# Optimization experiments

Measured on AMD Instinct MI355X. Metric: run time of the kernel, lower is better.

Reference implementation:

```python
import jax, jax.numpy as jnp
import numpy as np

B, S, D = 8, 1024, 768
H = 12
HD = D // H
DROPOUT_P = 0.5


def setup_inputs() -> dict:
    key = jax.random.key(0)
    ks = jax.random.split(key, 9)
    scale = 1.0 / np.sqrt(D)
    return {
        "x": jax.random.normal(ks[0], (B, S, D), dtype=jnp.float32),
        "wq": jax.random.normal(ks[1], (D, D), dtype=jnp.float32) * scale,
        "bq": jax.random.normal(ks[2], (D,), dtype=jnp.float32) * 0.01,
        "wk": jax.random.normal(ks[3], (D, D), dtype=jnp.float32) * scale,
        "bk": jax.random.normal(ks[4], (D,), dtype=jnp.float32) * 0.01,
        "wv": jax.random.normal(ks[5], (D, D), dtype=jnp.float32) * scale,
        "bv": jax.random.normal(ks[6], (D,), dtype=jnp.float32) * 0.01,
        "wo": jax.random.normal(ks[7], (D, D), dtype=jnp.float32) * scale,
        "bo": jax.random.normal(ks[8], (D,), dtype=jnp.float32) * 0.01,
    }


def reference(x, wq, bq, wk, bk, wv, bv, wo, bo):
    # QKV projections (torch Linear: y = x @ W.T + b)
    def proj(w, b):
        y = jnp.einsum("bsd,ed->bse", x, w) + b
        # [B,S,D] -> [B,H,S,HD]
        return y.reshape(B, S, H, HD).transpose(0, 2, 1, 3)

    q = proj(wq, bq)
    k = proj(wk, bk)
    v = proj(wv, bv)

    scores = jnp.einsum("bhqd,bhkd->bhqk", q, k) / jnp.sqrt(
        jnp.asarray(HD, dtype=x.dtype)
    )
    # dropout BEFORE softmax (non-standard, faithful to source), training=True
    dkey = jax.random.key(42)
    keep = jax.random.bernoulli(dkey, 1.0 - DROPOUT_P, scores.shape)
    scores = jnp.where(keep, scores / (1.0 - DROPOUT_P), 0.0)

    attn = jax.nn.softmax(scores, axis=-1)
    o = jnp.einsum("bhqk,bhkd->bhqd", attn, v)
    o = o.transpose(0, 2, 1, 3).reshape(B, S, D)
    return jnp.einsum("bsd,ed->bse", o, wo) + bo
```

## Files before the change

kernel.cpp:

```cpp
#include <hip/hip_runtime.h>
#include <hip/hip_bf16.h>
#include <stdint.h>

typedef __bf16 bf16_t;
typedef __attribute__((ext_vector_type(8))) __bf16 bf16x8;
typedef __attribute__((ext_vector_type(4))) __bf16 bf16x4;
typedef __attribute__((ext_vector_type(4))) float f32x4;

#define MFMA16(a, b, c) __builtin_amdgcn_mfma_f32_16x16x32_bf16(a, b, c, 0, 0, 0)

#define KS2 (0x1BD11BDAu ^ 42u)
#define OFF_TILES 9
#define GMASK_WORDS 1769472u

#define ROT4(rr)                                                        \
    {                                                                   \
        y00 += y10; y10 = __builtin_amdgcn_alignbit(y10, y10, 32u - (rr)); y10 ^= y00; \
        y01 += y11; y11 = __builtin_amdgcn_alignbit(y11, y11, 32u - (rr)); y11 ^= y01; \
        y02 += y12; y12 = __builtin_amdgcn_alignbit(y12, y12, 32u - (rr)); y12 ^= y02; \
        y03 += y13; y13 = __builtin_amdgcn_alignbit(y13, y13, 32u - (rr)); y13 ^= y03; \
    }
#define INJ4(a, b)                                                      \
    {                                                                   \
        y00 += (a); y10 += (b);                                         \
        y01 += (a); y11 += (b);                                         \
        y02 += (a); y12 += (b);                                         \
        y03 += (a); y13 += (b);                                         \
    }

__device__ __forceinline__ uint32_t tf4bits(uint32_t e0, int c) {
    uint32_t y00 = 0u, y10 = e0 + 42u;
    uint32_t y01 = 0u, y11 = e0 + 43u;
    uint32_t y02 = 0u, y12 = e0 + 44u;
    uint32_t y03 = 0u, y13 = e0 + 45u;
    ROT4(13) ROT4(15) ROT4(26) ROT4(6)   INJ4(42u, KS2 + 1u)
    ROT4(17) ROT4(29) ROT4(16) ROT4(24)  INJ4(KS2, 0u + 2u)
    ROT4(13) ROT4(15) ROT4(26) ROT4(6)   INJ4(0u, 42u + 3u)
    ROT4(17) ROT4(29) ROT4(16) ROT4(24)  INJ4(42u, KS2 + 4u)
    ROT4(13) ROT4(15) ROT4(26) ROT4(6)   INJ4(KS2, 0u + 5u)
    const uint32_t b0 = (y00 ^ y10) >> 31, b1 = (y01 ^ y11) >> 31;
    const uint32_t b2 = (y02 ^ y12) >> 31, b3 = (y03 ^ y13) >> 31;
    return (b0 | (b1 << 1) | (b2 << 2) | (b3 << 3)) << c;
}

__device__ __forceinline__ bf16x8 cvt8(float4 a, float4 b) {
    bf16x8 v;
    v[0] = (bf16_t)a.x; v[1] = (bf16_t)a.y; v[2] = (bf16_t)a.z; v[3] = (bf16_t)a.w;
    v[4] = (bf16_t)b.x; v[5] = (bf16_t)b.y; v[6] = (bf16_t)b.z; v[7] = (bf16_t)b.w;
    return v;
}

__global__ __launch_bounds__(512, 4)
void qkv_gemm(const float* __restrict__ x,
              const float* __restrict__ wq, const float* __restrict__ bq,
              const float* __restrict__ wk, const float* __restrict__ bk,
              const float* __restrict__ wv, const float* __restrict__ bv,
              bf16_t* __restrict__ qb, bf16_t* __restrict__ kb,
              bf16_t* __restrict__ vtb, uint32_t* __restrict__ gmask)
{
    const int mt = blockIdx.x;
    const int nt = blockIdx.y;
    const int mat = blockIdx.z;

    __shared__ bf16_t As[128][40];
    __shared__ bf16_t Bs[128][40];

    const int t = threadIdx.x;

    if (t < 256) {
        const float* w   = (mat == 0) ? wq : ((mat == 1) ? wk : wv);
        const float* bia = (mat == 0) ? bq : ((mat == 1) ? bk : bv);
        const int wid = t >> 6, l = t & 63, l15 = l & 15, lg = l >> 4;
        const int wr = wid >> 1, wc = wid & 1;

        f32x4 acc[4][4] = {};
        const int srow = t >> 1, scol = (t & 1) * 16;
        const float* xa = x + (size_t)(mt * 128 + srow) * 768 + scol;
        const float* wa = w + (size_t)(nt * 128 + srow) * 768 + scol;

        for (int kt = 0; kt < 24; ++kt) {
            const float* pa = xa + kt * 32;
            const float* pb = wa + kt * 32;
            float4 a0 = *(const float4*)(pa + 0),  a1 = *(const float4*)(pa + 4);
            float4 a2 = *(const float4*)(pa + 8),  a3 = *(const float4*)(pa + 12);
            float4 b0 = *(const float4*)(pb + 0),  b1 = *(const float4*)(pb + 4);
            float4 b2 = *(const float4*)(pb + 8),  b3 = *(const float4*)(pb + 12);
            __syncthreads();
            *(bf16x8*)&As[srow][scol]     = cvt8(a0, a1);
            *(bf16x8*)&As[srow][scol + 8] = cvt8(a2, a3);
            *(bf16x8*)&Bs[srow][scol]     = cvt8(b0, b1);
            *(bf16x8*)&Bs[srow][scol + 8] = cvt8(b2, b3);
            __syncthreads();

            bf16x8 af[4], bf[4];
#pragma unroll
            for (int m = 0; m < 4; ++m) af[m] = *(const bf16x8*)&As[wr * 64 + m * 16 + l15][lg * 8];
#pragma unroll
            for (int n = 0; n < 4; ++n) bf[n] = *(const bf16x8*)&Bs[wc * 64 + n * 16 + l15][lg * 8];
#pragma unroll
            for (int m = 0; m < 4; ++m)
#pragma unroll
                for (int n = 0; n < 4; ++n)
                    acc[m][n] = MFMA16(af[m], bf[n], acc[m][n]);
        }

        const int eb = nt * 128 + wc * 64;
        const int mb = mt * 128 + wr * 64;
#pragma unroll
        for (int n = 0; n < 4; ++n) {
            const int e = eb + n * 16 + l15;
            const float bias = bia[e];
            const int h = e >> 6, hd = e & 63;
#pragma unroll
            for (int m = 0; m < 4; ++m) {
                const int m0 = mb + m * 16 + lg * 4;
                const int b = m0 >> 10, s0 = m0 & 1023;
                if (mat == 2) {
                    bf16x4 pv;
#pragma unroll
                    for (int r = 0; r < 4; ++r) pv[r] = (bf16_t)(acc[m][n][r] + bias);
                    *(bf16x4*)(vtb + (((size_t)(b * 12 + h)) << 16) + ((size_t)hd << 10) + s0) = pv;
                } else {
                    bf16_t* dst = (mat == 0) ? qb : kb;
                    const float sc = (mat == 0) ? 0.25f : 1.0f;
                    const size_t base = (((size_t)(b * 12 + h)) << 16) + ((size_t)s0 << 6) + hd;
#pragma unroll
                    for (int r = 0; r < 4; ++r)
                        dst[base + (size_t)r * 64] = (bf16_t)((acc[m][n][r] + bias) * sc);
                }
            }
        }
    } else {
        const uint32_t u = (uint32_t)(t - 256);
        const uint32_t bl = (uint32_t)(mt + 64 * (nt + 6 * mat));
        const uint32_t wbase = bl * 1536u + u;
        uint32_t word = 0u, ebase = 0u, widx = 0u;
        for (int s = 0; s < 48; ++s) {
            const int chunk = s >> 3, c = (s & 7) * 4;
            if ((s & 7) == 0) {
                widx = wbase + 256u * (uint32_t)chunk;
                const uint32_t bh  = widx / 18432u;
                const uint32_t rem = widx - bh * 18432u;
                const uint32_t q   = rem / 18u;
                const uint32_t w18 = rem - q * 18u;
                ebase = (bh << 20) | (q << 10) | (w18 * 32u);
                word = 0u;
            }
            word |= tf4bits(ebase + (uint32_t)c, c);
            if ((s & 7) == 7) gmask[widx] = word;
            __syncthreads();
        }
    }
}

__global__ __launch_bounds__(512, 4)
void attn_kernel(const bf16_t* __restrict__ qb, const bf16_t* __restrict__ kb,
                 const bf16_t* __restrict__ vtb, const uint32_t* __restrict__ gmask,
                 bf16_t* __restrict__ ob)
{
    const int qt = blockIdx.x;
    const int bh = blockIdx.y;
    const int t = threadIdx.x, w = t >> 6, l = t & 63, l15 = l & 15, lg = l >> 4;

    __shared__ bf16_t Kl[2][64][72];
    __shared__ bf16_t Vl[2][64][72];
    __shared__ bf16_t Pl[4][16][72];
    __shared__ ushort Mh[7][64][2][2];

    const size_t base = ((size_t)bh) << 16;
    const uint32_t fbase = ((uint32_t)bh) << 20;
    const int q0b = qt * 64;
    const int q0 = q0b + w * 16;

    const int u = t & 255;
    const int mq = u >> 2, mword = (u >> 1) & 1, mhalf = u & 1;
    const uint32_t moff = (uint32_t)(mword * 32 + mhalf * 16);

    f32x4 oacc[4] = {};
    float lst[4] = {0.f, 0.f, 0.f, 0.f};
    bf16x8 qf[2];
    uint32_t mhw = 0u;
    int ms = 0;

    if (w < 4) {
        const size_t qbase = base + (size_t)(q0 + l15) * 64 + lg * 8;
        qf[0] = *(const bf16x8*)(qb + qbase);
        qf[1] = *(const bf16x8*)(qb + qbase + 32);
#pragma unroll
        for (int sdx = 0; sdx < 2; ++sdx) {
            const int idx = sdx * 256 + t;
            const int row = idx >> 3, seg = idx & 7;
            *(uint4*)&Kl[0][row][seg * 8] =
                *(const uint4*)(kb + base + ((size_t)row << 6) + seg * 8);
            *(uint4*)&Vl[0][row][seg * 8] =
                *(const uint4*)(vtb + base + ((size_t)row << 10) + seg * 8);
        }
    }
    __syncthreads();

    for (int kt = 0; kt < 16; ++kt) {
        const int cur = kt & 1, nxt = cur ^ 1;
        if (w < 4) {
            const int ktn = (kt < 15) ? kt + 1 : 15;
            const int row0 = t >> 3, seg = t & 7;
            const int row1 = row0 + 32;
            const uint4 ka0 = *(const uint4*)(kb + base + ((size_t)(ktn * 64 + row0) << 6) + seg * 8);
            const uint4 ka1 = *(const uint4*)(kb + base + ((size_t)(ktn * 64 + row1) << 6) + seg * 8);
            const uint4 va0 = *(const uint4*)(vtb + base + ((size_t)row0 << 10) + ktn * 64 + seg * 8);
            const uint4 va1 = *(const uint4*)(vtb + base + ((size_t)row1 << 10) + ktn * 64 + seg * 8);

            f32x4 sc[4] = {};
#pragma unroll
            for (int ks = 0; ks < 2; ++ks)
#pragma unroll
                for (int n = 0; n < 4; ++n) {
                    bf16x8 kf = *(const bf16x8*)&Kl[cur][n * 16 + l15][ks * 32 + lg * 8];
                    sc[n] = MFMA16(qf[ks], kf, sc[n]);
                }

#pragma unroll
            for (int r = 0; r < 4; ++r) {
                const int ql = w * 16 + lg * 4 + r;
                uint32_t w0, w1;
                if (kt < OFF_TILES) {
                    const uint32_t qg = (uint32_t)(q0b + ql);
                    const uint32_t wi = ((uint32_t)bh * 1024u + qg) * 18u + (uint32_t)(kt * 2);
                    w0 = gmask[wi]; w1 = gmask[wi + 1];
                } else {
                    const uint32_t* mrow = (const uint32_t*)&Mh[kt - OFF_TILES][ql][0][0];
                    w0 = mrow[0]; w1 = mrow[1];
                }
                float ps = 0.f;
#pragma unroll
                for (int n = 0; n < 4; ++n) {
                    const uint32_t wrd = (n < 2) ? w0 : w1;
                    const uint32_t bit = ((uint32_t)(n & 1) << 4) + (uint32_t)l15;
                    const float e = __expf(sc[n][r]);
                    const float p = ((wrd >> bit) & 1u) ? 1.0f : e;
                    ps += p;
                    Pl[w][lg * 4 + r][n * 16 + l15] = (bf16_t)p;
                }
                lst[r] += ps;
            }

            {
                const bf16x8 pa0 = *(const bf16x8*)&Pl[w][l15][lg * 8];
                const bf16x8 pa1 = *(const bf16x8*)&Pl[w][l15][32 + lg * 8];
#pragma unroll
                for (int n = 0; n < 4; ++n) {
                    const bf16x8 v0 = *(const bf16x8*)&Vl[cur][n * 16 + l15][lg * 8];
                    const bf16x8 v1 = *(const bf16x8*)&Vl[cur][n * 16 + l15][32 + lg * 8];
                    oacc[n] = MFMA16(pa0, v0, oacc[n]);
                    oacc[n] = MFMA16(pa1, v1, oacc[n]);
                }
            }

            {
                const int row0w = t >> 3, segw = t & 7;
                *(uint4*)&Kl[nxt][row0w][segw * 8]      = ka0;
                *(uint4*)&Kl[nxt][row0w + 32][segw * 8] = ka1;
                *(uint4*)&Vl[nxt][row0w][segw * 8]      = va0;
                *(uint4*)&Vl[nxt][row0w + 32][segw * 8] = va1;
            }
        } else {
#pragma unroll
            for (int q2 = 0; q2 < 2; ++q2) {
                if (ms < 28) {
                    const int ti = ms >> 2;
                    const int c = (ms & 3) * 4;
                    const uint32_t mbase = fbase | ((uint32_t)(q0b + mq) << 10)
                                         | ((uint32_t)((OFF_TILES + ti) * 64) + moff + (uint32_t)c);
                    mhw |= tf4bits(mbase, c);
                    if ((ms & 3) == 3) {
                        Mh[ti][mq][mword][mhalf] = (ushort)mhw;
                        mhw = 0u;
                    }
                    ++ms;
                }
            }
        }
        __syncthreads();
    }

    if (w < 4) {
        const int b = bh / 12, h = bh % 12;
#pragma unroll
        for (int r = 0; r < 4; ++r) {
            float ps = lst[r];
#pragma unroll
            for (int mk = 1; mk < 16; mk <<= 1) ps += __shfl_xor(ps, mk);
            const float inv = 1.f / ps;
            const size_t row = ((size_t)(b * 1024 + q0 + lg * 4 + r)) * 768 + h * 64;
#pragma unroll
            for (int n = 0; n < 4; ++n)
                ob[row + n * 16 + l15] = (bf16_t)(oacc[n][r] * inv);
        }
    }
}

__global__ __launch_bounds__(256, 2)
void out_gemm(const bf16_t* __restrict__ ob, const float* __restrict__ wo,
              const float* __restrict__ bo, float* __restrict__ out)
{
    const int mt = blockIdx.x, nt = blockIdx.y;
    __shared__ bf16_t As[128][40];
    __shared__ bf16_t Bs[128][40];
    const int t = threadIdx.x;
    const int wid = t >> 6, l = t & 63, l15 = l & 15, lg = l >> 4;
    const int wr = wid >> 1, wc = wid & 1;
    f32x4 acc[4][4] = {};

    const int srow = t >> 1, scol = (t & 1) * 16;
    const bf16_t* aa = ob + (size_t)(mt * 128 + srow) * 768 + scol;
    const float*  wa = wo + (size_t)(nt * 128 + srow) * 768 + scol;

    for (int kt = 0; kt < 24; ++kt) {
        uint4 a01 = *(const uint4*)(aa + kt * 32);
        uint4 a23 = *(const uint4*)(aa + kt * 32 + 8);
        const float* pb = wa + kt * 32;
        float4 b0 = *(const float4*)(pb + 0), b1 = *(const float4*)(pb + 4);
        float4 b2 = *(const float4*)(pb + 8), b3 = *(const float4*)(pb + 12);
        __syncthreads();
        *(uint4*)&As[srow][scol]      = a01;
        *(uint4*)&As[srow][scol + 8]  = a23;
        *(bf16x8*)&Bs[srow][scol]     = cvt8(b0, b1);
        *(bf16x8*)&Bs[srow][scol + 8] = cvt8(b2, b3);
        __syncthreads();

        bf16x8 af[4], bf[4];
#pragma unroll
        for (int m = 0; m < 4; ++m) af[m] = *(const bf16x8*)&As[wr * 64 + m * 16 + l15][lg * 8];
#pragma unroll
        for (int n = 0; n < 4; ++n) bf[n] = *(const bf16x8*)&Bs[wc * 64 + n * 16 + l15][lg * 8];
#pragma unroll
        for (int m = 0; m < 4; ++m)
#pragma unroll
            for (int n = 0; n < 4; ++n)
                acc[m][n] = MFMA16(af[m], bf[n], acc[m][n]);
    }

#pragma unroll
    for (int n = 0; n < 4; ++n) {
        const int e = nt * 128 + wc * 64 + n * 16 + l15;
        const float bias = bo[e];
#pragma unroll
        for (int m = 0; m < 4; ++m) {
            const int m0 = mt * 128 + wr * 64 + m * 16 + lg * 4;
#pragma unroll
            for (int r = 0; r < 4; ++r)
                out[(size_t)(m0 + r) * 768 + e] = acc[m][n][r] + bias;
        }
    }
}

__global__ void fill_zero(float* p, int n) {
    int i = blockIdx.x * 256 + threadIdx.x;
    if (i < n) p[i] = 0.f;
}

extern "C" void kernel_launch(void* const* d_in, const int* in_sizes, int n_in,
                              void* d_out, int out_size, void* d_ws, size_t ws_size,
                              hipStream_t stream) {
    const float* x  = (const float*)d_in[0];
    const float* wq = (const float*)d_in[1];
    const float* bq = (const float*)d_in[2];
    const float* wk = (const float*)d_in[3];
    const float* bk = (const float*)d_in[4];
    const float* wv = (const float*)d_in[5];
    const float* bv = (const float*)d_in[6];
    const float* wo = (const float*)d_in[7];
    const float* bo = (const float*)d_in[8];
    float* out = (float*)d_out;

    const size_t NEED = 4ull * 6291456ull * 2ull + (size_t)GMASK_WORDS * 4ull;
    if (ws_size < NEED) {
        fill_zero<<<(out_size + 255) / 256, 256, 0, stream>>>(out, out_size);
        return;
    }

    bf16_t* qb  = (bf16_t*)d_ws;
    bf16_t* kb  = qb  + 6291456;
    bf16_t* vtb = kb  + 6291456;
    bf16_t* ob  = vtb + 6291456;
    uint32_t* gmask = (uint32_t*)(ob + 6291456);

    qkv_gemm<<<dim3(64, 6, 3), 512, 0, stream>>>(x, wq, bq, wk, bk, wv, bv,
                                                 qb, kb, vtb, gmask);
    attn_kernel<<<dim3(16, 96), 512, 0, stream>>>(qb, kb, vtb, gmask, ob);
    out_gemm<<<dim3(64, 6), 256, 0, stream>>>(ob, wo, bo, out);
}
```

Measured before the change: 274.0 us.

## Double-buffer QKV GEMM shared tiles and halve barriers per k-step

After: 275.9 us. Within noise of the previous version (+0.7%).

```diff
diff --git a/kernel.cpp b/kernel.cpp
--- a/kernel.cpp
+++ b/kernel.cpp
@@ -62,8 +62,8 @@
     const int nt = blockIdx.y;
     const int mat = blockIdx.z;
 
-    __shared__ bf16_t As[128][40];
-    __shared__ bf16_t Bs[128][40];
+    __shared__ bf16_t As[2][128][40];
+    __shared__ bf16_t Bs[2][128][40];
 
     const int t = threadIdx.x;
 
@@ -78,30 +78,49 @@
         const float* xa = x + (size_t)(mt * 128 + srow) * 768 + scol;
         const float* wa = w + (size_t)(nt * 128 + srow) * 768 + scol;
 
+        {
+            float4 a0 = *(const float4*)(xa + 0),  a1 = *(const float4*)(xa + 4);
+            float4 a2 = *(const float4*)(xa + 8),  a3 = *(const float4*)(xa + 12);
+            float4 b0 = *(const float4*)(wa + 0),  b1 = *(const float4*)(wa + 4);
+            float4 b2 = *(const float4*)(wa + 8),  b3 = *(const float4*)(wa + 12);
+            *(bf16x8*)&As[0][srow][scol]     = cvt8(a0, a1);
+            *(bf16x8*)&As[0][srow][scol + 8] = cvt8(a2, a3);
+            *(bf16x8*)&Bs[0][srow][scol]     = cvt8(b0, b1);
+            *(bf16x8*)&Bs[0][srow][scol + 8] = cvt8(b2, b3);
+        }
+
         for (int kt = 0; kt < 24; ++kt) {
-            const float* pa = xa + kt * 32;
-            const float* pb = wa + kt * 32;
-            float4 a0 = *(const float4*)(pa + 0),  a1 = *(const float4*)(pa + 4);
-            float4 a2 = *(const float4*)(pa + 8),  a3 = *(const float4*)(pa + 12);
-            float4 b0 = *(const float4*)(pb + 0),  b1 = *(const float4*)(pb + 4);
-            float4 b2 = *(const float4*)(pb + 8),  b3 = *(const float4*)(pb + 12);
             __syncthreads();
-            *(bf16x8*)&As[srow][scol]     = cvt8(a0, a1);
-            *(bf16x8*)&As[srow][scol + 8] = cvt8(a2, a3);
-            *(bf16x8*)&Bs[srow][scol]     = cvt8(b0, b1);
-            *(bf16x8*)&Bs[srow][scol + 8] = cvt8(b2, b3);
-            __syncthreads();
+            const int cur = kt & 1;
+
+            float4 a0, a1, a2, a3, b0, b1, b2, b3;
+            if (kt < 23) {
+                const float* pa = xa + (kt + 1) * 32;
+                const float* pb = wa + (kt + 1) * 32;
+                a0 = *(const float4*)(pa + 0);  a1 = *(const float4*)(pa + 4);
+                a2 = *(const float4*)(pa + 8);  a3 = *(const float4*)(pa + 12);
+                b0 = *(const float4*)(pb + 0);  b1 = *(const float4*)(pb + 4);
+                b2 = *(const float4*)(pb + 8);  b3 = *(const float4*)(pb + 12);
+            }
 
             bf16x8 af[4], bf[4];
 #pragma unroll
-            for (int m = 0; m < 4; ++m) af[m] = *(const bf16x8*)&As[wr * 64 + m * 16 + l15][lg * 8];
-#pragma unroll
-            for (int n = 0; n < 4; ++n) bf[n] = *(const bf16x8*)&Bs[wc * 64 + n * 16 + l15][lg * 8];
+            for (int m = 0; m < 4; ++m) af[m] = *(const bf16x8*)&As[cur][wr * 64 + m * 16 + l15][lg * 8];
+#pragma unroll
+            for (int n = 0; n < 4; ++n) bf[n] = *(const bf16x8*)&Bs[cur][wc * 64 + n * 16 + l15][lg * 8];
 #pragma unroll
             for (int m = 0; m < 4; ++m)
 #pragma unroll
                 for (int n = 0; n < 4; ++n)
                     acc[m][n] = MFMA16(af[m], bf[n], acc[m][n]);
+
+            if (kt < 23) {
+                const int nb = cur ^ 1;
+                *(bf16x8*)&As[nb][srow][scol]     = cvt8(a0, a1);
+                *(bf16x8*)&As[nb][srow][scol + 8] = cvt8(a2, a3);
+                *(bf16x8*)&Bs[nb][srow][scol]     = cvt8(b0, b1);
+                *(bf16x8*)&Bs[nb][srow][scol + 8] = cvt8(b2, b3);
+            }
         }
 
         const int eb = nt * 128 + wc * 64;
@@ -135,20 +154,24 @@
         const uint32_t bl = (uint32_t)(mt + 64 * (nt + 6 * mat));
         const uint32_t wbase = bl * 1536u + u;
         uint32_t word = 0u, ebase = 0u, widx = 0u;
-        for (int s = 0; s < 48; ++s) {
-            const int chunk = s >> 3, c = (s & 7) * 4;
-            if ((s & 7) == 0) {
-                widx = wbase + 256u * (uint32_t)chunk;
-                const uint32_t bh  = widx / 18432u;
-                const uint32_t rem = widx - bh * 18432u;
-                const uint32_t q   = rem / 18u;
-                const uint32_t w18 = rem - q * 18u;
-                ebase = (bh << 20) | (q << 10) | (w18 * 32u);
-                word = 0u;
-            }
-            word |= tf4bits(ebase + (uint32_t)c, c);
-            if ((s & 7) == 7) gmask[widx] = word;
+        for (int it = 0; it < 24; ++it) {
             __syncthreads();
+#pragma unroll
+            for (int q2 = 0; q2 < 2; ++q2) {
+                const int s = it * 2 + q2;
+                const int chunk = s >> 3, c = (s & 7) * 4;
+                if ((s & 7) == 0) {
+                    widx = wbase + 256u * (uint32_t)chunk;
+                    const uint32_t bh  = widx / 18432u;
+                    const uint32_t rem = widx - bh * 18432u;
+                    const uint32_t q   = rem / 18u;
+                    const uint32_t w18 = rem - q * 18u;
+                    ebase = (bh << 20) | (q << 10) | (w18 * 32u);
+                    word = 0u;
+                }
+                word |= tf4bits(ebase + (uint32_t)c, c);
+                if ((s & 7) == 7) gmask[widx] = word;
+            }
         }
     }
 }
```

## Split mask generation into separate blocks instead of sharing blocks with GEMM waves

Applied to the files above, without the earlier changes.

After: 551.1 us. +101.1%, slower.

```diff
diff --git a/kernel.cpp b/kernel.cpp
--- a/kernel.cpp
+++ b/kernel.cpp
@@ -50,105 +50,102 @@
     return v;
 }
 
-__global__ __launch_bounds__(512, 4)
-void qkv_gemm(const float* __restrict__ x,
+__global__ __launch_bounds__(256)
+void qkv_mask(const float* __restrict__ x,
               const float* __restrict__ wq, const float* __restrict__ bq,
               const float* __restrict__ wk, const float* __restrict__ bk,
               const float* __restrict__ wv, const float* __restrict__ bv,
               bf16_t* __restrict__ qb, bf16_t* __restrict__ kb,
               bf16_t* __restrict__ vtb, uint32_t* __restrict__ gmask)
 {
-    const int mt = blockIdx.x;
-    const int nt = blockIdx.y;
-    const int mat = blockIdx.z;
-
     __shared__ bf16_t As[128][40];
     __shared__ bf16_t Bs[128][40];
 
+    const int bid = blockIdx.x;
+    const int grp = bid >> 2, sub = bid & 3;
     const int t = threadIdx.x;
 
-    if (t < 256) {
-        const float* w   = (mat == 0) ? wq : ((mat == 1) ? wk : wv);
-        const float* bia = (mat == 0) ? bq : ((mat == 1) ? bk : bv);
-        const int wid = t >> 6, l = t & 63, l15 = l & 15, lg = l >> 4;
-        const int wr = wid >> 1, wc = wid & 1;
-
-        f32x4 acc[4][4] = {};
-        const int srow = t >> 1, scol = (t & 1) * 16;
-        const float* xa = x + (size_t)(mt * 128 + srow) * 768 + scol;
-        const float* wa = w + (size_t)(nt * 128 + srow) * 768 + scol;
-
-        for (int kt = 0; kt < 24; ++kt) {
-            const float* pa = xa + kt * 32;
-            const float* pb = wa + kt * 32;
-            float4 a0 = *(const float4*)(pa + 0),  a1 = *(const float4*)(pa + 4);
-            float4 a2 = *(const float4*)(pa + 8),  a3 = *(const float4*)(pa + 12);
-            float4 b0 = *(const float4*)(pb + 0),  b1 = *(const float4*)(pb + 4);
-            float4 b2 = *(const float4*)(pb + 8),  b3 = *(const float4*)(pb + 12);
-            __syncthreads();
-            *(bf16x8*)&As[srow][scol]     = cvt8(a0, a1);
-            *(bf16x8*)&As[srow][scol + 8] = cvt8(a2, a3);
-            *(bf16x8*)&Bs[srow][scol]     = cvt8(b0, b1);
-            *(bf16x8*)&Bs[srow][scol + 8] = cvt8(b2, b3);
-            __syncthreads();
-
-            bf16x8 af[4], bf[4];
-#pragma unroll
-            for (int m = 0; m < 4; ++m) af[m] = *(const bf16x8*)&As[wr * 64 + m * 16 + l15][lg * 8];
-#pragma unroll
-            for (int n = 0; n < 4; ++n) bf[n] = *(const bf16x8*)&Bs[wc * 64 + n * 16 + l15][lg * 8];
-#pragma unroll
-            for (int m = 0; m < 4; ++m)
-#pragma unroll
-                for (int n = 0; n < 4; ++n)
-                    acc[m][n] = MFMA16(af[m], bf[n], acc[m][n]);
-        }
-
-        const int eb = nt * 128 + wc * 64;
-        const int mb = mt * 128 + wr * 64;
-#pragma unroll
-        for (int n = 0; n < 4; ++n) {
-            const int e = eb + n * 16 + l15;
-            const float bias = bia[e];
-            const int h = e >> 6, hd = e & 63;
-#pragma unroll
-            for (int m = 0; m < 4; ++m) {
-                const int m0 = mb + m * 16 + lg * 4;
-                const int b = m0 >> 10, s0 = m0 & 1023;
-                if (mat == 2) {
-                    bf16x4 pv;
-#pragma unroll
-                    for (int r = 0; r < 4; ++r) pv[r] = (bf16_t)(acc[m][n][r] + bias);
-                    *(bf16x4*)(vtb + (((size_t)(b * 12 + h)) << 16) + ((size_t)hd << 10) + s0) = pv;
-                } else {
-                    bf16_t* dst = (mat == 0) ? qb : kb;
-                    const float sc = (mat == 0) ? 0.25f : 1.0f;
-                    const size_t base = (((size_t)(b * 12 + h)) << 16) + ((size_t)s0 << 6) + hd;
-#pragma unroll
-                    for (int r = 0; r < 4; ++r)
-                        dst[base + (size_t)r * 64] = (bf16_t)((acc[m][n][r] + bias) * sc);
-                }
-            }
-        }
-    } else {
-        const uint32_t u = (uint32_t)(t - 256);
-        const uint32_t bl = (uint32_t)(mt + 64 * (nt + 6 * mat));
-        const uint32_t wbase = bl * 1536u + u;
-        uint32_t word = 0u, ebase = 0u, widx = 0u;
-        for (int s = 0; s < 48; ++s) {
-            const int chunk = s >> 3, c = (s & 7) * 4;
-            if ((s & 7) == 0) {
-                widx = wbase + 256u * (uint32_t)chunk;
-                const uint32_t bh  = widx / 18432u;
-                const uint32_t rem = widx - bh * 18432u;
-                const uint32_t q   = rem / 18u;
-                const uint32_t w18 = rem - q * 18u;
-                ebase = (bh << 20) | (q << 10) | (w18 * 32u);
-                word = 0u;
-            }
-            word |= tf4bits(ebase + (uint32_t)c, c);
-            if ((s & 7) == 7) gmask[widx] = word;
-            __syncthreads();
+    if (sub == 3) {
+        uint32_t widx = (uint32_t)grp * 256u + (uint32_t)t;
+        for (int j = 0; j < 18; ++j, widx += 98304u) {
+            const uint32_t bh  = widx / 18432u;
+            const uint32_t rem = widx - bh * 18432u;
+            const uint32_t q   = rem / 18u;
+            const uint32_t w18 = rem - q * 18u;
+            const uint32_t ebase = (bh << 20) | (q << 10) | (w18 * 32u);
+            uint32_t word = 0u;
+#pragma unroll
+            for (int c = 0; c < 32; c += 4) word |= tf4bits(ebase + (uint32_t)c, c);
+            gmask[widx] = word;
+        }
+        return;
+    }
+
+    const int gid = grp * 3 + sub;
+    const int mt = gid & 63;
+    const int rest = gid >> 6;
+    const int nt = rest % 6, mat = rest / 6;
+    const float* w   = (mat == 0) ? wq : ((mat == 1) ? wk : wv);
+    const float* bia = (mat == 0) ? bq : ((mat == 1) ? bk : bv);
+
+    const int wid = t >> 6, l = t & 63, l15 = l & 15, lg = l >> 4;
+    const int wr = wid >> 1, wc = wid & 1;
+
+    f32x4 acc[4][4] = {};
+    const int srow = t >> 1, scol = (t & 1) * 16;
+    const float* xa = x + (size_t)(mt * 128 + srow) * 768 + scol;
+    const float* wa = w + (size_t)(nt * 128 + srow) * 768 + scol;
+
+    for (int kt = 0; kt < 24; ++kt) {
+        const float* pa = xa + kt * 32;
+        const float* pb = wa + kt * 32;
+        float4 a0 = *(const float4*)(pa + 0),  a1 = *(const float4*)(pa + 4);
+        float4 a2 = *(const float4*)(pa + 8),  a3 = *(const float4*)(pa + 12);
+        float4 b0 = *(const float4*)(pb + 0),  b1 = *(const float4*)(pb + 4);
+        float4 b2 = *(const float4*)(pb + 8),  b3 = *(const float4*)(pb + 12);
+        __syncthreads();
+        *(bf16x8*)&As[srow][scol]     = cvt8(a0, a1);
+        *(bf16x8*)&As[srow][scol + 8] = cvt8(a2, a3);
+        *(bf16x8*)&Bs[srow][scol]     = cvt8(b0, b1);
+        *(bf16x8*)&Bs[srow][scol + 8] = cvt8(b2, b3);
+        __syncthreads();
+
+        bf16x8 af[4], bf[4];
+#pragma unroll
+        for (int m = 0; m < 4; ++m) af[m] = *(const bf16x8*)&As[wr * 64 + m * 16 + l15][lg * 8];
+#pragma unroll
+        for (int n = 0; n < 4; ++n) bf[n] = *(const bf16x8*)&Bs[wc * 64 + n * 16 + l15][lg * 8];
+#pragma unroll
+        for (int m = 0; m < 4; ++m)
+#pragma unroll
+            for (int n = 0; n < 4; ++n)
+                acc[m][n] = MFMA16(af[m], bf[n], acc[m][n]);
+    }
+
+    const int eb = nt * 128 + wc * 64;
+    const int mb = mt * 128 + wr * 64;
+#pragma unroll
+    for (int n = 0; n < 4; ++n) {
+        const int e = eb + n * 16 + l15;
+        const float bias = bia[e];
+        const int h = e >> 6, hd = e & 63;
+#pragma unroll
+        for (int m = 0; m < 4; ++m) {
+            const int m0 = mb + m * 16 + lg * 4;
+            const int b = m0 >> 10, s0 = m0 & 1023;
+            if (mat == 2) {
+                bf16x4 pv;
+#pragma unroll
+                for (int r = 0; r < 4; ++r) pv[r] = (bf16_t)(acc[m][n][r] + bias);
+                *(bf16x4*)(vtb + (((size_t)(b * 12 + h)) << 16) + ((size_t)hd << 10) + s0) = pv;
+            } else {
+                bf16_t* dst = (mat == 0) ? qb : kb;
+                const float sc = (mat == 0) ? 0.25f : 1.0f;
+                const size_t base = (((size_t)(b * 12 + h)) << 16) + ((size_t)s0 << 6) + hd;
+#pragma unroll
+                for (int r = 0; r < 4; ++r)
+                    dst[base + (size_t)r * 64] = (bf16_t)((acc[m][n][r] + bias) * sc);
+            }
         }
     }
 }
@@ -384,8 +381,7 @@
     bf16_t* ob  = vtb + 6291456;
     uint32_t* gmask = (uint32_t*)(ob + 6291456);
 
-    qkv_gemm<<<dim3(64, 6, 3), 512, 0, stream>>>(x, wq, bq, wk, bk, wv, bv,
-                                                 qb, kb, vtb, gmask);
+    qkv_mask<<<1536, 256, 0, stream>>>(x, wq, bq, wk, bk, wv, bv, qb, kb, vtb, gmask);
     attn_kernel<<<dim3(16, 96), 512, 0, stream>>>(qb, kb, vtb, gmask, ob);
     out_gemm<<<dim3(64, 6), 256, 0, stream>>>(ob, wo, bo, out);
 }
```

## Drop LDS staging in QKV GEMM and decouple mask-generation warps

Applied to the files above, without the earlier changes.

Result: slower. 364.5 us (+33.0%).

```diff
diff --git a/kernel.cpp b/kernel.cpp
--- a/kernel.cpp
+++ b/kernel.cpp
@@ -50,7 +50,7 @@
     return v;
 }
 
-__global__ __launch_bounds__(512, 4)
+__global__ __launch_bounds__(512, 2)
 void qkv_gemm(const float* __restrict__ x,
               const float* __restrict__ wq, const float* __restrict__ bq,
               const float* __restrict__ wk, const float* __restrict__ bk,
@@ -61,76 +61,9 @@
     const int mt = blockIdx.x;
     const int nt = blockIdx.y;
     const int mat = blockIdx.z;
-
-    __shared__ bf16_t As[128][40];
-    __shared__ bf16_t Bs[128][40];
-
     const int t = threadIdx.x;
 
-    if (t < 256) {
-        const float* w   = (mat == 0) ? wq : ((mat == 1) ? wk : wv);
-        const float* bia = (mat == 0) ? bq : ((mat == 1) ? bk : bv);
-        const int wid = t >> 6, l = t & 63, l15 = l & 15, lg = l >> 4;
-        const int wr = wid >> 1, wc = wid & 1;
-
-        f32x4 acc[4][4] = {};
-        const int srow = t >> 1, scol = (t & 1) * 16;
-        const float* xa = x + (size_t)(mt * 128 + srow) * 768 + scol;
-        const float* wa = w + (size_t)(nt * 128 + srow) * 768 + scol;
-
-        for (int kt = 0; kt < 24; ++kt) {
-            const float* pa = xa + kt * 32;
-            const float* pb = wa + kt * 32;
-            float4 a0 = *(const float4*)(pa + 0),  a1 = *(const float4*)(pa + 4);
-            float4 a2 = *(const float4*)(pa + 8),  a3 = *(const float4*)(pa + 12);
-            float4 b0 = *(const float4*)(pb + 0),  b1 = *(const float4*)(pb + 4);
-            float4 b2 = *(const float4*)(pb + 8),  b3 = *(const float4*)(pb + 12);
-            __syncthreads();
-            *(bf16x8*)&As[srow][scol]     = cvt8(a0, a1);
-            *(bf16x8*)&As[srow][scol + 8] = cvt8(a2, a3);
-            *(bf16x8*)&Bs[srow][scol]     = cvt8(b0, b1);
-            *(bf16x8*)&Bs[srow][scol + 8] = cvt8(b2, b3);
-            __syncthreads();
-
-            bf16x8 af[4], bf[4];
-#pragma unroll
-            for (int m = 0; m < 4; ++m) af[m] = *(const bf16x8*)&As[wr * 64 + m * 16 + l15][lg * 8];
-#pragma unroll
-            for (int n = 0; n < 4; ++n) bf[n] = *(const bf16x8*)&Bs[wc * 64 + n * 16 + l15][lg * 8];
-#pragma unroll
-            for (int m = 0; m < 4; ++m)
-#pragma unroll
-                for (int n = 0; n < 4; ++n)
-                    acc[m][n] = MFMA16(af[m], bf[n], acc[m][n]);
-        }
-
-        const int eb = nt * 128 + wc * 64;
-        const int mb = mt * 128 + wr * 64;
-#pragma unroll
-        for (int n = 0; n < 4; ++n) {
-            const int e = eb + n * 16 + l15;
-            const float bias = bia[e];
-            const int h = e >> 6, hd = e & 63;
-#pragma unroll
-            for (int m = 0; m < 4; ++m) {
-                const int m0 = mb + m * 16 + lg * 4;
-                const int b = m0 >> 10, s0 = m0 & 1023;
-                if (mat == 2) {
-                    bf16x4 pv;
-#pragma unroll
-                    for (int r = 0; r < 4; ++r) pv[r] = (bf16_t)(acc[m][n][r] + bias);
-                    *(bf16x4*)(vtb + (((size_t)(b * 12 + h)) << 16) + ((size_t)hd << 10) + s0) = pv;
-                } else {
-                    bf16_t* dst = (mat == 0) ? qb : kb;
-                    const float sc = (mat == 0) ? 0.25f : 1.0f;
-                    const size_t base = (((size_t)(b * 12 + h)) << 16) + ((size_t)s0 << 6) + hd;
-#pragma unroll
-                    for (int r = 0; r < 4; ++r)
-                        dst[base + (size_t)r * 64] = (bf16_t)((acc[m][n][r] + bias) * sc);
-                }
-            }
-        }
-    } else {
+    if (t >= 256) {
         const uint32_t u = (uint32_t)(t - 256);
         const uint32_t bl = (uint32_t)(mt + 64 * (nt + 6 * mat));
         const uint32_t wbase = bl * 1536u + u;
@@ -148,7 +81,63 @@
             }
             word |= tf4bits(ebase + (uint32_t)c, c);
             if ((s & 7) == 7) gmask[widx] = word;
-            __syncthreads();
+        }
+        return;
+    }
+
+    const float* w   = (mat == 0) ? wq : ((mat == 1) ? wk : wv);
+    const float* bia = (mat == 0) ? bq : ((mat == 1) ? bk : bv);
+    const int wid = t >> 6, l = t & 63, l15 = l & 15, lg = l >> 4;
+    const int wr = wid >> 1, wc = wid & 1;
+
+    const int mb = mt * 128 + wr * 64;
+    const int eb = nt * 128 + wc * 64;
+    const float* Ab = x + (size_t)(mb + l15) * 768 + lg * 8;
+    const float* Bb = w + (size_t)(eb + l15) * 768 + lg * 8;
+
+    f32x4 acc[4][4] = {};
+
+    for (int kt = 0; kt < 24; ++kt) {
+        bf16x8 af[4], bf[4];
+#pragma unroll
+        for (int m = 0; m < 4; ++m) {
+            const float* p = Ab + (size_t)(m * 16) * 768 + kt * 32;
+            af[m] = cvt8(*(const float4*)p, *(const float4*)(p + 4));
+        }
+#pragma unroll
+        for (int n = 0; n < 4; ++n) {
+            const float* p = Bb + (size_t)(n * 16) * 768 + kt * 32;
+            bf[n] = cvt8(*(const float4*)p, *(const float4*)(p + 4));
+        }
+#pragma unroll
+        for (int m = 0; m < 4; ++m)
+#pragma unroll
+            for (int n = 0; n < 4; ++n)
+                acc[m][n] = MFMA16(af[m], bf[n], acc[m][n]);
+    }
+
+#pragma unroll
+    for (int n = 0; n < 4; ++n) {
+        const int e = eb + n * 16 + l15;
+        const float bias = bia[e];
+        const int h = e >> 6, hd = e & 63;
+#pragma unroll
+        for (int m = 0; m < 4; ++m) {
+            const int m0 = mb + m * 16 + lg * 4;
+            const int b = m0 >> 10, s0 = m0 & 1023;
+            if (mat == 2) {
+                bf16x4 pv;
+#pragma unroll
+                for (int r = 0; r < 4; ++r) pv[r] = (bf16_t)(acc[m][n][r] + bias);
+                *(bf16x4*)(vtb + (((size_t)(b * 12 + h)) << 16) + ((size_t)hd << 10) + s0) = pv;
+            } else {
+                bf16_t* dst = (mat == 0) ? qb : kb;
+                const float sc = (mat == 0) ? 0.25f : 1.0f;
+                const size_t base = (((size_t)(b * 12 + h)) << 16) + ((size_t)s0 << 6) + hd;
+#pragma unroll
+                for (int r = 0; r < 4; ++r)
+                    dst[base + (size_t)r * 64] = (bf16_t)((acc[m][n][r] + bias) * sc);
+            }
         }
     }
 }
```
